# Optimization experiments

Hardware: AMD Instinct MI355X
Metric: run time of the kernel (lower is better)

## Reference

```python
import jax, jax.numpy as jnp
import numpy as np

D_MODEL = 256
N_HEAD = 8
HEAD_DIM = D_MODEL // N_HEAD
N_TOTAL = 24576
B, T = 64, 512


def setup_inputs() -> dict:
    key = jax.random.key(0)
    ks = jax.random.split(key, 12)
    s = 1.0 / np.sqrt(D_MODEL)
    return {
        "x": jax.random.normal(ks[0], (N_TOTAL, D_MODEL), jnp.float32),
        "Wq": jax.random.uniform(ks[1], (D_MODEL, D_MODEL), jnp.float32, -s, s),
        "bq": jax.random.uniform(ks[2], (D_MODEL,), jnp.float32, -s, s),
        "Wk": jax.random.uniform(ks[3], (D_MODEL, D_MODEL), jnp.float32, -s, s),
        "bk": jax.random.uniform(ks[4], (D_MODEL,), jnp.float32, -s, s),
        "Wv": jax.random.uniform(ks[5], (D_MODEL, D_MODEL), jnp.float32, -s, s),
        "bv": jax.random.uniform(ks[6], (D_MODEL,), jnp.float32, -s, s),
        "Wp": jax.random.uniform(ks[7], (D_MODEL, D_MODEL), jnp.float32, -s, s),
        "bp": jax.random.uniform(ks[8], (D_MODEL,), jnp.float32, -s, s),
        "padpack_index": jax.random.randint(ks[9], (B, T), 0, N_TOTAL, jnp.int64 if jax.config.jax_enable_x64 else jnp.int32),
        "padpack_batch": jax.random.randint(ks[10], (B, T), 0, B, jnp.int32),
        "padpack_inverse_index": jax.random.randint(ks[11], (N_TOTAL,), 0, B * T, jnp.int64 if jax.config.jax_enable_x64 else jnp.int32),
    }


def reference(x, Wq, bq, Wk, bk, Wv, bv, Wp, bp, padpack_index, padpack_batch, padpack_inverse_index):
    # gather ragged tokens into packed [B, T, C]
    xp = x[padpack_index]
    # mask: True where packed slots share the same segment id (matches
    # original masked_fill(batch_i == batch_j, -1e9))
    mask = padpack_batch[:, :, None] == padpack_batch[:, None, :]  # [B,T,T]
    # QKV projections (torch Linear: x @ W.T + b), split heads
    def heads(w, b):
        h = xp @ w.T + b
        return h.reshape(B, T, N_HEAD, HEAD_DIM).transpose(0, 2, 1, 3)  # [B,H,T,D]
    q, k, v = heads(Wq, bq), heads(Wk, bk), heads(Wv, bv)
    att = jnp.einsum("bhtd,bhsd->bhts", q, k) * (1.0 / np.sqrt(HEAD_DIM))
    att = jnp.where(mask[:, None], jnp.float32(-1e9), att)
    att = jax.nn.softmax(att, axis=-1)
    y = jnp.einsum("bhts,bhsd->bhtd", att, v)  # [B,H,T,D]
    y = y.transpose(0, 2, 1, 3).reshape(B, T, D_MODEL)
    y = y @ Wp.T + bp
    # scatter back to ragged layout
    return y.reshape(B * T, D_MODEL)[padpack_inverse_index]
```

## Files before the change

kernel.cpp:

```cpp
#include <hip/hip_runtime.h>


typedef __attribute__((ext_vector_type(8))) short short8;
typedef __attribute__((ext_vector_type(4))) float f32x4;

#define N_TOTAL 24576
#define B_ 64
#define T_ 512
#define DM 256
#define NH 8
#define HD 32
#define F3 768

#define QSCALE 0.25503463f
#define VSP 514

__device__ __forceinline__ unsigned short f2bf(float f) {
  unsigned int u = __float_as_uint(f);
  u += 0x7fffu + ((u >> 16) & 1u);
  return (unsigned short)(u >> 16);
}

__device__ __forceinline__ void gl_lds16(const void* g, void* l) {
  __builtin_amdgcn_global_load_lds(
      (const __attribute__((address_space(1))) unsigned int*)g,
      (__attribute__((address_space(3))) unsigned int*)l, 16, 0, 0);
}

__global__ __launch_bounds__(256) void pack_kernel(
    const float* __restrict__ x, const float* __restrict__ Wq,
    const float* __restrict__ Wk, const float* __restrict__ Wv,
    const float* __restrict__ Wp, const float* __restrict__ bq,
    const float* __restrict__ bk, const float* __restrict__ bv,
    const int* __restrict__ idx,
    short* __restrict__ XP, short* __restrict__ WCAT, short* __restrict__ WPb,
    float* __restrict__ BCAT) {
  int gid = blockIdx.x * 256 + threadIdx.x;
  if (gid < 768)
    BCAT[gid] = (gid < 256) ? bq[gid] : (gid < 512 ? bk[gid - 256] : bv[gid - 512]);
  const float* src;
  short* dst;
  if (gid < 1048576) {
    int row = gid >> 5, seg = gid & 31;
    src = x + (size_t)idx[row] * DM + seg * 8;
    dst = XP + (size_t)gid * 8;
  } else if (gid < 1073152) {
    int u = gid - 1048576;
    int f = u >> 5, seg = u & 31;
    const float* W = (f < 256) ? Wq : ((f < 512) ? Wk : Wv);
    src = W + (size_t)(f & 255) * DM + seg * 8;
    dst = WCAT + (size_t)u * 8;
  } else {
    int u = gid - 1073152;
    src = Wp + (size_t)u * 8;
    dst = WPb + (size_t)u * 8;
  }
  const float4* s4 = (const float4*)src;
  float4 a = s4[0], b = s4[1];
  short8 o;
  o[0] = (short)f2bf(a.x); o[1] = (short)f2bf(a.y);
  o[2] = (short)f2bf(a.z); o[3] = (short)f2bf(a.w);
  o[4] = (short)f2bf(b.x); o[5] = (short)f2bf(b.y);
  o[6] = (short)f2bf(b.z); o[7] = (short)f2bf(b.w);
  *(short8*)dst = o;
}

__global__ __launch_bounds__(256) void qkv_gemm(
    const short* __restrict__ XP, const short* __restrict__ WCAT,
    const float* __restrict__ BCAT, unsigned short* __restrict__ QKVp) {
  __shared__ __align__(16) char smem[3 * 16384];
  int tid = threadIdx.x;
  int lane = tid & 63, w = tid >> 6;
  int i = lane & 15, q = lane >> 4;
  int m0 = blockIdx.x * 128, n0 = blockIdx.y * 128;
  int wm = (w & 1) * 64, wn = (w >> 1) * 64;
  int csa = q ^ ((i >> 1) & 3);

  f32x4 zf = {0.f, 0.f, 0.f, 0.f};
  f32x4 acc[4][4];
#pragma unroll
  for (int mt = 0; mt < 4; mt++)
#pragma unroll
    for (int nt = 0; nt < 4; nt++) acc[mt][nt] = zf;

  auto stage = [&](int k, int s) {
#pragma unroll
    for (int p = 0; p < 2; p++) {
      int U = p * 256 + tid;
      int row = U >> 2, c = U & 3;
      int cs = c ^ ((row >> 1) & 3);
      gl_lds16(XP + (size_t)(m0 + row) * DM + k * 32 + cs * 8,
               smem + s * 16384 + U * 16);
      gl_lds16(WCAT + (size_t)(n0 + row) * DM + k * 32 + cs * 8,
               smem + s * 16384 + 8192 + U * 16);
    }
  };

  stage(0, 0);
  stage(1, 1);
#pragma unroll
  for (int k = 0; k < 8; k++) {
    if (k == 7)
      asm volatile("s_waitcnt vmcnt(0) lgkmcnt(0)\ns_barrier" ::: "memory");
    else
      asm volatile("s_waitcnt vmcnt(4) lgkmcnt(0)\ns_barrier" ::: "memory");
    const short* Asb = (const short*)(smem + (k % 3) * 16384);
    const short* Bsb = Asb + 4096;
    short8 a[4], bfr[4];
#pragma unroll
    for (int mt = 0; mt < 4; mt++)
      a[mt] = *(const short8*)&Asb[(wm + mt * 16 + i) * 32 + csa * 8];
#pragma unroll
    for (int nt = 0; nt < 4; nt++)
      bfr[nt] = *(const short8*)&Bsb[(wn + nt * 16 + i) * 32 + csa * 8];
    if (k < 6) stage(k + 2, (k + 2) % 3);
#pragma unroll
    for (int mt = 0; mt < 4; mt++)
#pragma unroll
      for (int nt = 0; nt < 4; nt++)
        acc[mt][nt] = __builtin_amdgcn_mfma_f32_16x16x32_bf16(a[mt], bfr[nt], acc[mt][nt], 0, 0, 0);
  }

  float scale = (n0 < 256) ? QSCALE : 1.0f;
#pragma unroll
  for (int nt = 0; nt < 4; nt++) {
    int f = n0 + wn + nt * 16 + i;
    float bias = BCAT[f];
#pragma unroll
    for (int mt = 0; mt < 4; mt++) {
#pragma unroll
      for (int r = 0; r < 4; r++) {
        int token = m0 + wm + mt * 16 + q * 4 + r;
        QKVp[(size_t)token * F3 + f] = f2bf((acc[mt][nt][r] + bias) * scale);
      }
    }
  }
}

__global__ __launch_bounds__(512) void attn_kernel(
    const unsigned short* __restrict__ QKVp, const int* __restrict__ batch,
    unsigned short* __restrict__ Y) {
  __shared__ __align__(16) short Vl[HD * VSP];
  __shared__ __align__(16) short pscr[8][64 * 40];
  __shared__ int sbat[T_];
  int tid = threadIdx.x, w = tid >> 6, lane = tid & 63;
  int i = lane & 15, q = lane >> 4;
  int bx = blockIdx.x;
  int h = bx >> 6, b = bx & 63;
  int t0 = w * 64;
  const unsigned short* Tok = QKVp + (size_t)b * T_ * F3;

  sbat[tid] = batch[b * T_ + tid];

  {
    int seg = tid & 3, sb = tid >> 2;
#pragma unroll
    for (int l = 0; l < 4; l++) {
      int s = sb + l * 128;
      short8 v = *(const short8*)&Tok[(size_t)s * F3 + 512 + h * HD + seg * 8];
#pragma unroll
      for (int j = 0; j < 8; j++) Vl[(seg * 8 + j) * VSP + s] = v[j];
    }
  }
  __syncthreads();

  short* pw = &pscr[w][0];

  short8 qf[4];
  int btv[4][4];
#pragma unroll
  for (int mt = 0; mt < 4; mt++)
    qf[mt] = *(const short8*)&Tok[(size_t)(t0 + mt * 16 + i) * F3 + h * HD + q * 8];
#pragma unroll
  for (int mt = 0; mt < 4; mt++) {
    int4 t4 = *(int4*)&sbat[t0 + mt * 16 + q * 4];
    btv[mt][0] = t4.x; btv[mt][1] = t4.y; btv[mt][2] = t4.z; btv[mt][3] = t4.w;
  }

  unsigned short ob = (i == 0) ? (unsigned short)0x3F80 : (unsigned short)0;
  short8 ones = {(short)ob, (short)ob, (short)ob, (short)ob,
                 (short)ob, (short)ob, (short)ob, (short)ob};

  f32x4 zf = {0.f, 0.f, 0.f, 0.f};
  f32x4 o[4][2], lacc[4];
#pragma unroll
  for (int mt = 0; mt < 4; mt++) {
    o[mt][0] = zf; o[mt][1] = zf; lacc[mt] = zf;
  }

  const unsigned short* Kcol = Tok + 256 + h * HD + q * 8;
  short8 k0f = *(const short8*)&Kcol[(size_t)(2 * i) * F3];
  short8 k1f = *(const short8*)&Kcol[(size_t)(2 * i + 1) * F3];
  int bs0 = sbat[2 * i], bs1 = sbat[2 * i + 1];

  for (int s0 = 0; s0 < T_; s0 += 32) {
    short8 ck0 = k0f, ck1 = k1f;
    int cb0 = bs0, cb1 = bs1;
    if (s0 + 32 < T_) {
      k0f = *(const short8*)&Kcol[(size_t)(s0 + 32 + 2 * i) * F3];
      k1f = *(const short8*)&Kcol[(size_t)(s0 + 32 + 2 * i + 1) * F3];
      bs0 = sbat[s0 + 32 + 2 * i];
      bs1 = sbat[s0 + 32 + 2 * i + 1];
    }
    short8 v0f = *(const short8*)&Vl[i * VSP + s0 + q * 8];
    short8 v1f = *(const short8*)&Vl[(16 + i) * VSP + s0 + q * 8];
#pragma unroll
    for (int mt = 0; mt < 4; mt++) {
      f32x4 st0 = __builtin_amdgcn_mfma_f32_16x16x32_bf16(qf[mt], ck0, zf, 0, 0, 0);
      f32x4 st1 = __builtin_amdgcn_mfma_f32_16x16x32_bf16(qf[mt], ck1, zf, 0, 0, 0);
#pragma unroll
      for (int r = 0; r < 4; r++) {
        float m0v = (btv[mt][r] == cb0) ? -1e9f : st0[r];
        float m1v = (btv[mt][r] == cb1) ? -1e9f : st1[r];
        unsigned e0 = __float_as_uint(__builtin_amdgcn_exp2f(m0v));
        unsigned e1 = __float_as_uint(__builtin_amdgcn_exp2f(m1v));
        unsigned pk = __builtin_amdgcn_perm(e1, e0, 0x07060302u);
        *(unsigned*)&pw[(mt * 16 + q * 4 + r) * 40 + 2 * i] = pk;
      }
    }
#pragma unroll
    for (int mt = 0; mt < 4; mt++) {
      short8 pa = *(short8*)&pw[(mt * 16 + i) * 40 + q * 8];
      o[mt][0] = __builtin_amdgcn_mfma_f32_16x16x32_bf16(pa, v0f, o[mt][0], 0, 0, 0);
      o[mt][1] = __builtin_amdgcn_mfma_f32_16x16x32_bf16(pa, v1f, o[mt][1], 0, 0, 0);
      lacc[mt] = __builtin_amdgcn_mfma_f32_16x16x32_bf16(pa, ones, lacc[mt], 0, 0, 0);
    }
  }

#pragma unroll
  for (int mt = 0; mt < 4; mt++) {
#pragma unroll
    for (int r = 0; r < 4; r++) {
      float lv = __shfl(lacc[mt][r], lane & 48, 64);
      float inv = __builtin_amdgcn_rcpf(lv);
      size_t yb = ((size_t)b * T_ + t0 + mt * 16 + q * 4 + r) * DM + h * HD;
      Y[yb + i] = f2bf(o[mt][0][r] * inv);
      Y[yb + 16 + i] = f2bf(o[mt][1][r] * inv);
    }
  }
}

__global__ __launch_bounds__(256) void out_gemm(
    const short* __restrict__ Y, const short* __restrict__ WPb,
    const float* __restrict__ bp, const int* __restrict__ inv,
    float* __restrict__ out) {
  __shared__ __align__(16) char smem[3 * 16384];
  int tid = threadIdx.x;
  int lane = tid & 63, w = tid >> 6;
  int i = lane & 15, q = lane >> 4;
  int m0 = blockIdx.x * 128, n0 = blockIdx.y * 128;
  int wm = (w & 1) * 64, wn = (w >> 1) * 64;
  int csa = q ^ ((i >> 1) & 3);

  int iv0 = inv[m0 + (tid >> 2)];
  int iv1 = inv[m0 + 64 + (tid >> 2)];

  f32x4 zf = {0.f, 0.f, 0.f, 0.f};
  f32x4 acc[4][4];
#pragma unroll
  for (int mt = 0; mt < 4; mt++)
#pragma unroll
    for (int nt = 0; nt < 4; nt++) acc[mt][nt] = zf;

  auto stage = [&](int k, int s) {
#pragma unroll
    for (int p = 0; p < 2; p++) {
      int U = p * 256 + tid;
      int row = U >> 2, c = U & 3;
      int cs = c ^ ((row >> 1) & 3);
      int iv = p ? iv1 : iv0;
      gl_lds16(Y + (size_t)iv * DM + k * 32 + cs * 8, smem + s * 16384 + U * 16);
      gl_lds16(WPb + (size_t)(n0 + row) * DM + k * 32 + cs * 8,
               smem + s * 16384 + 8192 + U * 16);
    }
  };

  stage(0, 0);
  stage(1, 1);
#pragma unroll
  for (int k = 0; k < 8; k++) {
    if (k == 7)
      asm volatile("s_waitcnt vmcnt(0) lgkmcnt(0)\ns_barrier" ::: "memory");
    else
      asm volatile("s_waitcnt vmcnt(4) lgkmcnt(0)\ns_barrier" ::: "memory");
    const short* Asb = (const short*)(smem + (k % 3) * 16384);
    const short* Bsb = Asb + 4096;
    short8 a[4], bfr[4];
#pragma unroll
    for (int mt = 0; mt < 4; mt++)
      a[mt] = *(const short8*)&Asb[(wm + mt * 16 + i) * 32 + csa * 8];
#pragma unroll
    for (int nt = 0; nt < 4; nt++)
      bfr[nt] = *(const short8*)&Bsb[(wn + nt * 16 + i) * 32 + csa * 8];
    if (k < 6) stage(k + 2, (k + 2) % 3);
#pragma unroll
    for (int mt = 0; mt < 4; mt++)
#pragma unroll
      for (int nt = 0; nt < 4; nt++)
        acc[mt][nt] = __builtin_amdgcn_mfma_f32_16x16x32_bf16(a[mt], bfr[nt], acc[mt][nt], 0, 0, 0);
  }

#pragma unroll
  for (int nt = 0; nt < 4; nt++) {
    int f = n0 + wn + nt * 16 + i;
    float bias = bp[f];
#pragma unroll
    for (int mt = 0; mt < 4; mt++) {
#pragma unroll
      for (int r = 0; r < 4; r++) {
        int row = m0 + wm + mt * 16 + q * 4 + r;
        out[(size_t)row * DM + f] = acc[mt][nt][r] + bias;
      }
    }
  }
}

extern "C" void kernel_launch(void* const* d_in, const int* in_sizes, int n_in,
                              void* d_out, int out_size, void* d_ws, size_t ws_size,
                              hipStream_t stream) {
  const float* x = (const float*)d_in[0];
  const float* Wq = (const float*)d_in[1];
  const float* bq = (const float*)d_in[2];
  const float* Wk = (const float*)d_in[3];
  const float* bk = (const float*)d_in[4];
  const float* Wv = (const float*)d_in[5];
  const float* bv = (const float*)d_in[6];
  const float* Wp = (const float*)d_in[7];
  const float* bp = (const float*)d_in[8];
  const int* idx = (const int*)d_in[9];
  const int* batch = (const int*)d_in[10];
  const int* inv = (const int*)d_in[11];
  float* out = (float*)d_out;

  char* ws = (char*)d_ws;
  short* XP = (short*)(ws + 0);
  short* WCAT = (short*)(ws + 16777216);
  short* WPb = (short*)(ws + 17170432);
  float* BCAT = (float*)(ws + 17301504);
  unsigned short* QKVp = (unsigned short*)(ws + 17304576);
  unsigned short* Yb = (unsigned short*)(ws + 67636224);

  pack_kernel<<<4224, 256, 0, stream>>>(x, Wq, Wk, Wv, Wp, bq, bk, bv, idx,
                                        XP, WCAT, WPb, BCAT);
  qkv_gemm<<<dim3(256, 6), 256, 0, stream>>>(XP, WCAT, BCAT, QKVp);
  attn_kernel<<<512, 512, 0, stream>>>(QKVp, batch, Yb);
  out_gemm<<<dim3(192, 2), 256, 0, stream>>>((const short*)Yb, WPb, bp, inv, out);
}
```

Before: 168.6 us.

## Keep attention probabilities in registers via transposed S MFMA and permlane swaps

Computes S transposed (K as the A operand, Q as B) so each lane holds scores along the key dimension. Cross-lane v_permlane32/16_swap instructions then rearrange the packed bf16 probabilities directly into the A-operand layout for the PV MFMA. This removes the per-wave LDS scratch round trip (write then read of P) and its shared memory. Launch bounds also request 4 blocks per CU. The risks are register pressure from the occupancy hint and correctness of the hand-written permlane fragment mapping.

```diff
diff --git a/kernel.cpp b/kernel.cpp
--- a/kernel.cpp
+++ b/kernel.cpp
@@ -137,11 +137,10 @@
   }
 }
 
-__global__ __launch_bounds__(512) void attn_kernel(
+__global__ __launch_bounds__(512, 4) void attn_kernel(
     const unsigned short* __restrict__ QKVp, const int* __restrict__ batch,
     unsigned short* __restrict__ Y) {
   __shared__ __align__(16) short Vl[HD * VSP];
-  __shared__ __align__(16) short pscr[8][64 * 40];
   __shared__ int sbat[T_];
   int tid = threadIdx.x, w = tid >> 6, lane = tid & 63;
   int i = lane & 15, q = lane >> 4;
@@ -164,18 +163,13 @@
   }
   __syncthreads();
 
-  short* pw = &pscr[w][0];
-
   short8 qf[4];
-  int btv[4][4];
+  int btm[4];
 #pragma unroll
   for (int mt = 0; mt < 4; mt++)
     qf[mt] = *(const short8*)&Tok[(size_t)(t0 + mt * 16 + i) * F3 + h * HD + q * 8];
 #pragma unroll
-  for (int mt = 0; mt < 4; mt++) {
-    int4 t4 = *(int4*)&sbat[t0 + mt * 16 + q * 4];
-    btv[mt][0] = t4.x; btv[mt][1] = t4.y; btv[mt][2] = t4.z; btv[mt][3] = t4.w;
-  }
+  for (int mt = 0; mt < 4; mt++) btm[mt] = sbat[t0 + mt * 16 + i];
 
   unsigned short ob = (i == 0) ? (unsigned short)0x3F80 : (unsigned short)0;
   short8 ones = {(short)ob, (short)ob, (short)ob, (short)ob,
@@ -188,39 +182,55 @@
     o[mt][0] = zf; o[mt][1] = zf; lacc[mt] = zf;
   }
 
-  const unsigned short* Kcol = Tok + 256 + h * HD + q * 8;
-  short8 k0f = *(const short8*)&Kcol[(size_t)(2 * i) * F3];
-  short8 k1f = *(const short8*)&Kcol[(size_t)(2 * i + 1) * F3];
-  int bs0 = sbat[2 * i], bs1 = sbat[2 * i + 1];
+  const unsigned short* Kb = Tok + 256 + h * HD + q * 8;
+  short8 k0f = *(const short8*)&Kb[(size_t)(i)*F3];
+  short8 k1f = *(const short8*)&Kb[(size_t)(16 + i) * F3];
 
   for (int s0 = 0; s0 < T_; s0 += 32) {
     short8 ck0 = k0f, ck1 = k1f;
-    int cb0 = bs0, cb1 = bs1;
     if (s0 + 32 < T_) {
-      k0f = *(const short8*)&Kcol[(size_t)(s0 + 32 + 2 * i) * F3];
-      k1f = *(const short8*)&Kcol[(size_t)(s0 + 32 + 2 * i + 1) * F3];
-      bs0 = sbat[s0 + 32 + 2 * i];
-      bs1 = sbat[s0 + 32 + 2 * i + 1];
-    }
+      k0f = *(const short8*)&Kb[(size_t)(s0 + 32 + i) * F3];
+      k1f = *(const short8*)&Kb[(size_t)(s0 + 48 + i) * F3];
+    }
+    int4 bs0 = *(const int4*)&sbat[s0 + q * 4];
+    int4 bs1 = *(const int4*)&sbat[s0 + 16 + q * 4];
     short8 v0f = *(const short8*)&Vl[i * VSP + s0 + q * 8];
     short8 v1f = *(const short8*)&Vl[(16 + i) * VSP + s0 + q * 8];
 #pragma unroll
     for (int mt = 0; mt < 4; mt++) {
-      f32x4 st0 = __builtin_amdgcn_mfma_f32_16x16x32_bf16(qf[mt], ck0, zf, 0, 0, 0);
-      f32x4 st1 = __builtin_amdgcn_mfma_f32_16x16x32_bf16(qf[mt], ck1, zf, 0, 0, 0);
-#pragma unroll
-      for (int r = 0; r < 4; r++) {
-        float m0v = (btv[mt][r] == cb0) ? -1e9f : st0[r];
-        float m1v = (btv[mt][r] == cb1) ? -1e9f : st1[r];
-        unsigned e0 = __float_as_uint(__builtin_amdgcn_exp2f(m0v));
-        unsigned e1 = __float_as_uint(__builtin_amdgcn_exp2f(m1v));
-        unsigned pk = __builtin_amdgcn_perm(e1, e0, 0x07060302u);
-        *(unsigned*)&pw[(mt * 16 + q * 4 + r) * 40 + 2 * i] = pk;
-      }
-    }
-#pragma unroll
-    for (int mt = 0; mt < 4; mt++) {
-      short8 pa = *(short8*)&pw[(mt * 16 + i) * 40 + q * 8];
+      f32x4 st0 = __builtin_amdgcn_mfma_f32_16x16x32_bf16(ck0, qf[mt], zf, 0, 0, 0);
+      f32x4 st1 = __builtin_amdgcn_mfma_f32_16x16x32_bf16(ck1, qf[mt], zf, 0, 0, 0);
+      int bm = btm[mt];
+      float e00 = __builtin_amdgcn_exp2f((bs0.x == bm) ? -1e9f : st0[0]);
+      float e01 = __builtin_amdgcn_exp2f((bs0.y == bm) ? -1e9f : st0[1]);
+      float e02 = __builtin_amdgcn_exp2f((bs0.z == bm) ? -1e9f : st0[2]);
+      float e03 = __builtin_amdgcn_exp2f((bs0.w == bm) ? -1e9f : st0[3]);
+      float e10 = __builtin_amdgcn_exp2f((bs1.x == bm) ? -1e9f : st1[0]);
+      float e11 = __builtin_amdgcn_exp2f((bs1.y == bm) ? -1e9f : st1[1]);
+      float e12 = __builtin_amdgcn_exp2f((bs1.z == bm) ? -1e9f : st1[2]);
+      float e13 = __builtin_amdgcn_exp2f((bs1.w == bm) ? -1e9f : st1[3]);
+      unsigned A0 = __builtin_amdgcn_perm(__float_as_uint(e01), __float_as_uint(e00), 0x07060302u);
+      unsigned A1 = __builtin_amdgcn_perm(__float_as_uint(e03), __float_as_uint(e02), 0x07060302u);
+      unsigned B0 = __builtin_amdgcn_perm(__float_as_uint(e11), __float_as_uint(e10), 0x07060302u);
+      unsigned B1 = __builtin_amdgcn_perm(__float_as_uint(e13), __float_as_uint(e12), 0x07060302u);
+      asm volatile(
+          "s_nop 1\n\t"
+          "v_permlane32_swap_b32 %0, %2\n\t"
+          "v_permlane32_swap_b32 %1, %3\n\t"
+          "s_nop 1\n\t"
+          "v_permlane16_swap_b32 %0, %2\n\t"
+          "v_permlane16_swap_b32 %1, %3\n\t"
+          "s_nop 1"
+          : "+v"(A0), "+v"(A1), "+v"(B0), "+v"(B1));
+      union {
+        unsigned u[4];
+        short8 s;
+      } cv;
+      cv.u[0] = A0;
+      cv.u[1] = A1;
+      cv.u[2] = B0;
+      cv.u[3] = B1;
+      short8 pa = cv.s;
       o[mt][0] = __builtin_amdgcn_mfma_f32_16x16x32_bf16(pa, v0f, o[mt][0], 0, 0, 0);
       o[mt][1] = __builtin_amdgcn_mfma_f32_16x16x32_bf16(pa, v1f, o[mt][1], 0, 0, 0);
       lacc[mt] = __builtin_amdgcn_mfma_f32_16x16x32_bf16(pa, ones, lacc[mt], 0, 0, 0);
```

Result: no change. 167.9 us (-0.4%).
